# Performance work log

Hardware: AMD Instinct MI355X
Metric: run time of the kernel (lower is better)

Reference implementation:

```python
import jax, jax.numpy as jnp
import numpy as np

MARGIN = 0.3
PD_EPS = 1e-6  # torch F.pairwise_distance adds eps to the difference


def setup_inputs() -> dict:
    key = jax.random.key(0)
    k1, k2 = jax.random.split(key)
    B, D, NUM_CLASSES = 8192, 256, 8
    embeddings = jax.random.normal(k1, (B, D), dtype=jnp.float32)
    labels = jax.random.randint(k2, (B,), 0, NUM_CLASSES, dtype=jnp.int64)
    return {"embeddings": embeddings, "labels": labels}


def _pairwise_euclidean(x):
    # cdist(x, x, p=2) via the Gram trick; clamp tiny negatives before sqrt
    sq = jnp.sum(x * x, axis=1)  # [B]
    d2 = sq[:, None] + sq[None, :] - 2.0 * (x @ x.T)
    return jnp.sqrt(jnp.maximum(d2, 0.0))


def reference(embeddings, labels):
    B = embeddings.shape[0]
    D = _pairwise_euclidean(embeddings)  # [B, B]

    eq = labels[:, None] == labels[None, :]
    eye = jnp.eye(B, dtype=bool)
    pos_mask = eq & ~eye          # same label, not self
    neg_mask = ~eq                # different label

    # hard mining: per anchor, farthest positive and closest negative
    pos_idx = jnp.argmax(jnp.where(pos_mask, D, -jnp.inf), axis=1)  # [B]
    neg_idx = jnp.argmin(jnp.where(neg_mask, D, jnp.inf), axis=1)   # [B]
    valid = pos_mask.any(axis=1) & neg_mask.any(axis=1)             # [B]

    # recompute triplet distances like F.pairwise_distance (eps on the diff)
    pos_dist = jnp.linalg.norm(embeddings - embeddings[pos_idx] + PD_EPS, axis=1)
    neg_dist = jnp.linalg.norm(embeddings - embeddings[neg_idx] + PD_EPS, axis=1)

    per_anchor = jax.nn.relu(pos_dist - neg_dist + MARGIN)
    n_valid = jnp.maximum(valid.sum(), 1)
    loss = jnp.sum(jnp.where(valid, per_anchor, 0.0)) / n_valid.astype(per_anchor.dtype)
    return loss
```

## Files before the change

kernel.cpp:

```cpp
#include <hip/hip_runtime.h>
#include <math.h>


typedef __attribute__((ext_vector_type(8))) short short8;
typedef __attribute__((ext_vector_type(4))) float floatx4;

#define B_N 8192
#define D_K 256

__device__ __forceinline__ unsigned short f2bf_rne(float f) {
  unsigned u = __float_as_uint(f);
  u += 0x7FFFu + ((u >> 16) & 1u);
  return (unsigned short)(u >> 16);
}

#define DPP_SHR(x, CTRL) \
  ((unsigned)__builtin_amdgcn_update_dpp((int)(x), (int)(x), (CTRL), 0xF, 0xF, false))

__global__ void k_hist(const int* __restrict__ lab, int* __restrict__ chunkhist) {
  __shared__ int h[8];
  const int tid = threadIdx.x, b = blockIdx.x;
  if (tid < 8) h[tid] = 0;
  __syncthreads();
  atomicAdd(&h[lab[b * 256 + tid] & 7], 1);
  __syncthreads();
  if (tid < 8) chunkhist[b * 8 + tid] = h[tid];
}

__global__ void k_perm(const int* __restrict__ lab, const int* __restrict__ chunkhist,
                       int* __restrict__ perm, int* __restrict__ labp) {
  __shared__ int ch[256];
  __shared__ int base[8];
  __shared__ int wcnt[4][8];
  const int tid = threadIdx.x, b = blockIdx.x;
  ch[tid] = chunkhist[tid];
  __syncthreads();
  if (tid < 8) {
    const int c = tid;
    int acc = 0;
    for (int cc = 0; cc < c; ++cc)
      for (int k = 0; k < 32; ++k) acc += ch[k * 8 + cc];
    for (int k = 0; k < b; ++k) acc += ch[k * 8 + c];
    base[c] = acc;
  }
  const int i    = b * 256 + tid;
  const int myc  = lab[i] & 7;
  const int lane = tid & 63, w = tid >> 6;
  unsigned long long bal[8];
#pragma unroll
  for (int c = 0; c < 8; ++c) bal[c] = __ballot(myc == c);
  if (lane == 0) {
#pragma unroll
    for (int c = 0; c < 8; ++c) wcnt[w][c] = (int)__popcll(bal[c]);
  }
  __syncthreads();
  int rank = (int)__popcll(bal[myc] & ((1ull << lane) - 1ull));
  for (int ww = 0; ww < w; ++ww) rank += wcnt[ww][myc];
  const int pos = base[myc] + rank;
  perm[pos] = i;
  labp[pos] = myc;
}

__global__ void k_split(const float* __restrict__ x, const int* __restrict__ perm,
                        unsigned short* __restrict__ xhf,
                        float* __restrict__ sqq,
                        float* __restrict__ sum, int* __restrict__ cnt,
                        int* __restrict__ done) {
  __shared__ float sw[64];
  const int tid  = threadIdx.x;
  const int lane = tid & 63;
  const int w    = tid >> 6;
  const int b    = blockIdx.x;
  const int m    = lane & 15;
  const int quad = lane >> 4;
  const int row  = b * 16 + m;
  const int rsrc = perm[row];

  float s = 0.f;
#pragma unroll
  for (int h = 0; h < 2; ++h) {
    int tk = w + h * 4;
    int kk = tk * 32 + quad * 8;
    float4 f0 = *reinterpret_cast<const float4*>(x + (size_t)rsrc * D_K + kk);
    float4 f1 = *reinterpret_cast<const float4*>(x + (size_t)rsrc * D_K + kk + 4);
    s += f0.x * f0.x + f0.y * f0.y + f0.z * f0.z + f0.w * f0.w;
    s += f1.x * f1.x + f1.y * f1.y + f1.z * f1.z + f1.w * f1.w;
    ushort4 lo, hi;
    lo.x = f2bf_rne(f0.x); lo.y = f2bf_rne(f0.y); lo.z = f2bf_rne(f0.z); lo.w = f2bf_rne(f0.w);
    hi.x = f2bf_rne(f1.x); hi.y = f2bf_rne(f1.y); hi.z = f2bf_rne(f1.z); hi.w = f2bf_rne(f1.w);
    size_t o = ((size_t)b * 8 + tk) * 512 + lane * 8;
    *reinterpret_cast<ushort4*>(xhf + o)     = lo;
    *reinterpret_cast<ushort4*>(xhf + o + 4) = hi;
  }
  s += __shfl_xor(s, 16);
  s += __shfl_xor(s, 32);
  if (quad == 0) sw[w * 16 + m] = s;
  __syncthreads();
  if (tid < 16) {
    int i = b * 16 + tid;
    float t = sw[tid] + sw[16 + tid] + sw[32 + tid] + sw[48 + tid];
    sqq[i] = fmaf(t, 128.f, 262144.f);
  }
  if (b == 0 && tid == 0) { *sum = 0.f; *cnt = 0; *done = 0; }
}

template <int MODE>
__device__ __forceinline__ void mine_tail(
    const floatx4* acc, const int* __restrict__ labp, const float* __restrict__ sqq,
    int i0, int bi, int bj, int w, int lane,
    unsigned* jbp, unsigned* jbn,
    unsigned* __restrict__ ppart, unsigned* __restrict__ npart) {
  const int wj = w & 1;
  const int quad = lane >> 4, l15 = lane & 15;

  float sqi[16];
#pragma unroll
  for (int r = 0; r < 16; ++r)
    sqi[r] = sqq[i0 + (r >> 2) * 16 + quad * 4 + (r & 3)];

  unsigned long long lip = 0ull;
  if (MODE == 2) {
#pragma unroll
    for (int r = 0; r < 16; ++r) {
      int ir = i0 + (r >> 2) * 16 + quad * 4 + (r & 3);
      lip |= (unsigned long long)((unsigned)labp[ir] & 0xFu) << (r * 4);
    }
  }

  unsigned pkey[16], nkey[16];
#pragma unroll
  for (int r = 0; r < 16; ++r) { pkey[r] = 0u; nkey[r] = 0xFFFFFFFFu; }

#pragma unroll
  for (int nt = 0; nt < 4; ++nt) {
    const int      j  = bj * 128 + wj * 64 + nt * 16 + l15;
    const float    sj = sqq[j];
    const unsigned jl = (MODE == 2) ? ((unsigned)labp[j] & 0xFu) : 0u;
    unsigned jp = 0u, jn = 0xFFFFFFFFu;
#pragma unroll
    for (int r = 0; r < 16; ++r) {
      float dot = acc[(r >> 2) * 4 + nt][r & 3];
      int   ir  = i0 + (r >> 2) * 16 + quad * 4 + (r & 3);
      unsigned keyi = ((unsigned)fmaf(-256.f, dot, sj) << 13) | (unsigned)j;
      unsigned keyj = ((unsigned)fmaf(-256.f, dot, sqi[r]) << 13) | (unsigned)ir;
      if (MODE == 2) {
        bool eq = (jl == (unsigned)((lip >> (r * 4)) & 0xFull));
        unsigned pci = eq ? keyi : 0u;
        unsigned nci = eq ? 0xFFFFFFFFu : keyi;
        pkey[r] = pkey[r] > pci ? pkey[r] : pci;
        nkey[r] = nkey[r] < nci ? nkey[r] : nci;
        unsigned pcj = eq ? keyj : 0u;
        unsigned ncj = eq ? 0xFFFFFFFFu : keyj;
        jp = jp > pcj ? jp : pcj;
        jn = jn < ncj ? jn : ncj;
      } else if (MODE == 1) {
        pkey[r] = pkey[r] > keyi ? pkey[r] : keyi;
        jp = jp > keyj ? jp : keyj;
      } else {
        nkey[r] = nkey[r] < keyi ? nkey[r] : keyi;
        jn = jn < keyj ? jn : keyj;
      }
    }
#pragma unroll
    for (int m = 16; m < 64; m <<= 1) {
      if (MODE != 0) { unsigned op = (unsigned)__shfl_xor((int)jp, m); jp = jp > op ? jp : op; }
      if (MODE != 1) { unsigned on = (unsigned)__shfl_xor((int)jn, m); jn = jn < on ? jn : on; }
    }
    if (quad == 0) {
      if (MODE != 0) jbp[w * 64 + nt * 16 + l15] = jp;
      if (MODE != 1) jbn[w * 64 + nt * 16 + l15] = jn;
    }
  }

#pragma unroll
  for (int r = 0; r < 16; ++r) {
    if (MODE != 0) { unsigned tp = DPP_SHR(pkey[r], 0x118); pkey[r] = pkey[r] > tp ? pkey[r] : tp; }
    if (MODE != 1) { unsigned tn = DPP_SHR(nkey[r], 0x118); nkey[r] = nkey[r] < tn ? nkey[r] : tn; }
  }
#pragma unroll
  for (int r = 0; r < 16; ++r) {
    if (MODE != 0) { unsigned tp = DPP_SHR(pkey[r], 0x114); pkey[r] = pkey[r] > tp ? pkey[r] : tp; }
    if (MODE != 1) { unsigned tn = DPP_SHR(nkey[r], 0x114); nkey[r] = nkey[r] < tn ? nkey[r] : tn; }
  }
#pragma unroll
  for (int r = 0; r < 16; ++r) {
    if (MODE != 0) { unsigned tp = DPP_SHR(pkey[r], 0x112); pkey[r] = pkey[r] > tp ? pkey[r] : tp; }
    if (MODE != 1) { unsigned tn = DPP_SHR(nkey[r], 0x112); nkey[r] = nkey[r] < tn ? nkey[r] : tn; }
  }
#pragma unroll
  for (int r = 0; r < 16; ++r) {
    if (MODE != 0) { unsigned tp = DPP_SHR(pkey[r], 0x111); pkey[r] = pkey[r] > tp ? pkey[r] : tp; }
    if (MODE != 1) { unsigned tn = DPP_SHR(nkey[r], 0x111); nkey[r] = nkey[r] < tn ? nkey[r] : tn; }
  }
#pragma unroll
  for (int r = 0; r < 16; ++r) {
    if (l15 == 15) {
      int ir = i0 + (r >> 2) * 16 + quad * 4 + (r & 3);
      size_t idx = (size_t)(2 * bj + wj) * B_N + ir;
      ppart[idx] = (MODE == 0) ? 0u : pkey[r];
      npart[idx] = (MODE == 1) ? 0xFFFFFFFFu : nkey[r];
    }
  }

  __syncthreads();
  if ((w >> 1) == 0 && bi != bj) {
    unsigned p = 0u, n = 0xFFFFFFFFu;
    if (MODE != 0) {
      p = jbp[w * 64 + lane];
      unsigned p2 = jbp[(w + 2) * 64 + lane];
      p = p > p2 ? p : p2;
    }
    if (MODE != 1) {
      n = jbn[w * 64 + lane];
      unsigned n2 = jbn[(w + 2) * 64 + lane];
      n = n < n2 ? n : n2;
    }
    int j = bj * 128 + wj * 64 + lane;
    size_t v = (size_t)(2 * bi + wj)       * B_N + j;
    size_t u = (size_t)(2 * bi + (1 - wj)) * B_N + j;
    ppart[v] = p;   npart[v] = n;
    ppart[u] = 0u;  npart[u] = 0xFFFFFFFFu;
  }
}

__global__ __launch_bounds__(256, 3) void k_mine16(
    const unsigned short* __restrict__ xhf, const int* __restrict__ labp,
    const float* __restrict__ sqq,
    unsigned* __restrict__ ppart, unsigned* __restrict__ npart) {
  __shared__ unsigned jbp[4 * 64], jbn[4 * 64];

  int t  = blockIdx.x;
  int bi = (int)(64.5f - sqrtf(64.5f * 64.5f - 2.f * (float)t));
  int b0 = 64 * bi - (bi * (bi - 1)) / 2;
  if (t < b0) { bi--; b0 = 64 * bi - (bi * (bi - 1)) / 2; }
  else {
    int b1 = 64 * (bi + 1) - ((bi + 1) * bi) / 2;
    if (t >= b1) { bi++; b0 = b1; }
  }
  const int bj = bi + (t - b0);

  const int tid  = threadIdx.x;
  const int lane = tid & 63;
  const int w    = tid >> 6;
  const int wi   = w >> 1;
  const int wj   = w & 1;
  const int i0   = bi * 128 + wi * 64;

  const int la0 = labp[bi * 128];
  const int la1 = labp[bi * 128 + 127];
  const int lb0 = labp[bj * 128];
  const int lb1 = labp[bj * 128 + 127];

  const unsigned aoff = (unsigned)(bi * 8 + wi * 4) * 4096u + (unsigned)lane * 8u;
  const unsigned boff = (unsigned)(bj * 8 + wj * 4) * 4096u + (unsigned)lane * 8u;

  floatx4 acc[16];
#pragma unroll
  for (int q = 0; q < 16; ++q) acc[q] = (floatx4)0.f;

#pragma unroll
  for (int tk = 0; tk < 8; ++tk) {
    short8 Bf[4];
#pragma unroll
    for (int nt = 0; nt < 4; ++nt)
      Bf[nt] = *reinterpret_cast<const short8*>(xhf + boff + (unsigned)(nt * 4096 + tk * 512));
    short8 Af[4];
#pragma unroll
    for (int mt = 0; mt < 4; ++mt)
      Af[mt] = *reinterpret_cast<const short8*>(xhf + aoff + (unsigned)(mt * 4096 + tk * 512));
#pragma unroll
    for (int mt = 0; mt < 4; ++mt)
#pragma unroll
      for (int nt = 0; nt < 4; ++nt)
        acc[mt * 4 + nt] = __builtin_amdgcn_mfma_f32_16x16x32_bf16(
            Af[mt], Bf[nt], acc[mt * 4 + nt], 0, 0, 0);
  }

  if (la1 < lb0 || lb1 < la0) {
    mine_tail<0>(acc, labp, sqq, i0, bi, bj, w, lane, jbp, jbn, ppart, npart);
  } else if (la0 == lb1 && la1 == lb0) {
    mine_tail<1>(acc, labp, sqq, i0, bi, bj, w, lane, jbp, jbn, ppart, npart);
  } else {
    mine_tail<2>(acc, labp, sqq, i0, bi, bj, w, lane, jbp, jbn, ppart, npart);
  }
}

__global__ void k_finish(const float* __restrict__ x, const int* __restrict__ perm,
                         const unsigned* __restrict__ ppart,
                         const unsigned* __restrict__ npart,
                         float* __restrict__ sum, int* __restrict__ cnt,
                         int* __restrict__ done, float* __restrict__ out) {
  __shared__ unsigned spk[32], snk[32];
  __shared__ float ssum[4];
  __shared__ int   scnt[4];
  const int tid = threadIdx.x;
  const int a0  = blockIdx.x * 32;

  if (tid < 32) { spk[tid] = 0u; snk[tid] = 0xFFFFFFFFu; }
  __syncthreads();

  {
    const int a    = a0 + (tid & 31);
    const int part = tid >> 5;
    unsigned p = 0u, n = 0xFFFFFFFFu;
#pragma unroll
    for (int s = 0; s < 16; ++s) {
      size_t idx = (size_t)(part * 16 + s) * B_N + a;
      unsigned pv = ppart[idx];
      unsigned nv = npart[idx];
      p = p > pv ? p : pv;
      n = n < nv ? n : nv;
    }
    atomicMax(&spk[tid & 31], p);
    atomicMin(&snk[tid & 31], n);
  }
  __syncthreads();

  const int w = tid >> 6, lane = tid & 63;
  float lsum = 0.f; int lcnt = 0;
#pragma unroll
  for (int it = 0; it < 8; ++it) {
    int al = w * 8 + it;
    int a  = a0 + al;
    unsigned p = spk[al];
    unsigned n = snk[al];
    bool valid = (p != 0u) && (n != 0xFFFFFFFFu);
    int  pidx = valid ? (int)(p & 8191u) : 0;
    int  nidx = valid ? (int)(n & 8191u) : 0;
    int  ra = perm[a], rp = perm[pidx], rn = perm[nidx];

    float4 xa = *reinterpret_cast<const float4*>(x + (size_t)ra * D_K + lane * 4);
    float4 xp = *reinterpret_cast<const float4*>(x + (size_t)rp * D_K + lane * 4);
    float4 xn = *reinterpret_cast<const float4*>(x + (size_t)rn * D_K + lane * 4);
    float dx, sp = 0.f, sn = 0.f;
    dx = xa.x - xp.x + 1e-6f; sp = fmaf(dx, dx, sp);
    dx = xa.y - xp.y + 1e-6f; sp = fmaf(dx, dx, sp);
    dx = xa.z - xp.z + 1e-6f; sp = fmaf(dx, dx, sp);
    dx = xa.w - xp.w + 1e-6f; sp = fmaf(dx, dx, sp);
    dx = xa.x - xn.x + 1e-6f; sn = fmaf(dx, dx, sn);
    dx = xa.y - xn.y + 1e-6f; sn = fmaf(dx, dx, sn);
    dx = xa.z - xn.z + 1e-6f; sn = fmaf(dx, dx, sn);
    dx = xa.w - xn.w + 1e-6f; sn = fmaf(dx, dx, sn);
#pragma unroll
    for (int o = 32; o > 0; o >>= 1) {
      sp += __shfl_down(sp, o, 64);
      sn += __shfl_down(sn, o, 64);
    }
    if (lane == 0 && valid) {
      float per = sqrtf(sp) - sqrtf(sn) + 0.3f;
      if (per > 0.f) lsum += per;
      lcnt += 1;
    }
  }
  if (lane == 0) { ssum[w] = lsum; scnt[w] = lcnt; }
  __syncthreads();
  if (tid == 0) {
    atomicAdd(sum, ssum[0] + ssum[1] + ssum[2] + ssum[3]);
    atomicAdd(cnt, scnt[0] + scnt[1] + scnt[2] + scnt[3]);
    __threadfence();
    int prev = atomicAdd(done, 1);
    if (prev == gridDim.x - 1) {
      float s = atomicAdd(sum, 0.f);
      int   cc = atomicAdd(cnt, 0);
      if (cc < 1) cc = 1;
      out[0] = s / (float)cc;
    }
  }
}

extern "C" void kernel_launch(void* const* d_in, const int* in_sizes, int n_in,
                              void* d_out, int out_size, void* d_ws, size_t ws_size,
                              hipStream_t stream) {
  const float* x   = (const float*)d_in[0];
  const int*   lab = (const int*)d_in[1];
  float*       out = (float*)d_out;

  char* ws = (char*)d_ws;
  unsigned short* xhf = (unsigned short*)ws;
  int* perm      = (int*)(ws + (size_t)4096 * 1024);
  int* labp      = (int*)(ws + (size_t)4096 * 1024 + 32768);
  int* chunkhist = (int*)(ws + (size_t)4096 * 1024 + 65536);
  float* sqq = (float*)(ws + (size_t)4608 * 1024);
  char*  pb = ws + (size_t)4608 * 1024 + 65536;
  size_t seg = (size_t)128 * B_N * 4;
  unsigned* ppart = (unsigned*)(pb);
  unsigned* npart = (unsigned*)(pb + seg);
  float* sum  = (float*)(pb + 2 * seg);
  int*   cnt  = (int*)(sum + 1);
  int*   done = (int*)(sum + 2);

  k_hist<<<32, 256, 0, stream>>>(lab, chunkhist);
  k_perm<<<32, 256, 0, stream>>>(lab, chunkhist, perm, labp);
  k_split<<<B_N / 16, 256, 0, stream>>>(x, perm, xhf, sqq, sum, cnt, done);
  k_mine16<<<2080, 256, 0, stream>>>(xhf, labp, sqq, ppart, npart);
  k_finish<<<B_N / 32, 256, 0, stream>>>(x, perm, ppart, npart, sum, cnt, done, out);
}
```

Baseline: 118.4 us.

## Merge sort kernels, halve partial buffers, reduce tile halves in LDS, swizzle blocks

Replaces the two-kernel histogram/permutation pass with a single 1024-thread block doing a counting sort, which saves one launch and moves the accumulator reset there. In the mining kernel, the per-wave row partial results are first combined across the two column halves in shared memory. Each tile then writes one partial per row instead of two, halving the ppart/npart buffers and the reads in k_finish. Block indices are also remapped with a stride-260 swizzle to spread triangular tiles across CUs. The extra LDS buffers and the added barrier-phase reduction cost a little occupancy, and the sort now runs serially on one block.

```diff
diff --git a/kernel.cpp b/kernel.cpp
--- a/kernel.cpp
+++ b/kernel.cpp
@@ -17,55 +17,67 @@
 #define DPP_SHR(x, CTRL) \
   ((unsigned)__builtin_amdgcn_update_dpp((int)(x), (int)(x), (CTRL), 0xF, 0xF, false))
 
-__global__ void k_hist(const int* __restrict__ lab, int* __restrict__ chunkhist) {
-  __shared__ int h[8];
-  const int tid = threadIdx.x, b = blockIdx.x;
-  if (tid < 8) h[tid] = 0;
-  __syncthreads();
-  atomicAdd(&h[lab[b * 256 + tid] & 7], 1);
-  __syncthreads();
-  if (tid < 8) chunkhist[b * 8 + tid] = h[tid];
-}
-
-__global__ void k_perm(const int* __restrict__ lab, const int* __restrict__ chunkhist,
-                       int* __restrict__ perm, int* __restrict__ labp) {
-  __shared__ int ch[256];
-  __shared__ int base[8];
-  __shared__ int wcnt[4][8];
-  const int tid = threadIdx.x, b = blockIdx.x;
-  ch[tid] = chunkhist[tid];
+__global__ __launch_bounds__(1024) void k_sort(const int* __restrict__ lab,
+                                               int* __restrict__ perm,
+                                               int* __restrict__ labp,
+                                               float* __restrict__ sum,
+                                               int* __restrict__ cnt,
+                                               int* __restrict__ done) {
+  __shared__ int wtot[16][8];
+  __shared__ int wbase[16][8];
+  __shared__ int ctot[8];
+  __shared__ int cbase[8];
+  const int tid = threadIdx.x, lane = tid & 63, w = tid >> 6;
+
+  int l[8], pre[8];
+  int lcnt[8] = {0, 0, 0, 0, 0, 0, 0, 0};
+#pragma unroll
+  for (int k = 0; k < 8; ++k) {
+    l[k] = lab[tid * 8 + k] & 7;
+    pre[k] = lcnt[l[k]]++;
+  }
+  int v[8];
+#pragma unroll
+  for (int c = 0; c < 8; ++c) v[c] = lcnt[c];
+  for (int d = 1; d < 64; d <<= 1) {
+#pragma unroll
+    for (int c = 0; c < 8; ++c) {
+      int t = __shfl_up(v[c], d, 64);
+      if (lane >= d) v[c] += t;
+    }
+  }
+  int lex[8];
+#pragma unroll
+  for (int c = 0; c < 8; ++c) lex[c] = v[c] - lcnt[c];
+  if (lane == 63) {
+#pragma unroll
+    for (int c = 0; c < 8; ++c) wtot[w][c] = v[c];
+  }
   __syncthreads();
   if (tid < 8) {
-    const int c = tid;
     int acc = 0;
-    for (int cc = 0; cc < c; ++cc)
-      for (int k = 0; k < 32; ++k) acc += ch[k * 8 + cc];
-    for (int k = 0; k < b; ++k) acc += ch[k * 8 + c];
-    base[c] = acc;
-  }
-  const int i    = b * 256 + tid;
-  const int myc  = lab[i] & 7;
-  const int lane = tid & 63, w = tid >> 6;
-  unsigned long long bal[8];
-#pragma unroll
-  for (int c = 0; c < 8; ++c) bal[c] = __ballot(myc == c);
-  if (lane == 0) {
-#pragma unroll
-    for (int c = 0; c < 8; ++c) wcnt[w][c] = (int)__popcll(bal[c]);
-  }
-  __syncthreads();
-  int rank = (int)__popcll(bal[myc] & ((1ull << lane) - 1ull));
-  for (int ww = 0; ww < w; ++ww) rank += wcnt[ww][myc];
-  const int pos = base[myc] + rank;
-  perm[pos] = i;
-  labp[pos] = myc;
+    for (int ww = 0; ww < 16; ++ww) { wbase[ww][tid] = acc; acc += wtot[ww][tid]; }
+    ctot[tid] = acc;
+  }
+  __syncthreads();
+  if (tid == 0) {
+    int acc = 0;
+    for (int c = 0; c < 8; ++c) { cbase[c] = acc; acc += ctot[c]; }
+    *sum = 0.f; *cnt = 0; *done = 0;
+  }
+  __syncthreads();
+#pragma unroll
+  for (int k = 0; k < 8; ++k) {
+    int c = l[k];
+    int pos = cbase[c] + wbase[w][c] + lex[c] + pre[k];
+    perm[pos] = tid * 8 + k;
+    labp[pos] = c;
+  }
 }
 
 __global__ void k_split(const float* __restrict__ x, const int* __restrict__ perm,
                         unsigned short* __restrict__ xhf,
-                        float* __restrict__ sqq,
-                        float* __restrict__ sum, int* __restrict__ cnt,
-                        int* __restrict__ done) {
+                        float* __restrict__ sqq) {
   __shared__ float sw[64];
   const int tid  = threadIdx.x;
   const int lane = tid & 63;
@@ -101,14 +113,13 @@
     float t = sw[tid] + sw[16 + tid] + sw[32 + tid] + sw[48 + tid];
     sqq[i] = fmaf(t, 128.f, 262144.f);
   }
-  if (b == 0 && tid == 0) { *sum = 0.f; *cnt = 0; *done = 0; }
 }
 
 template <int MODE>
 __device__ __forceinline__ void mine_tail(
     const floatx4* acc, const int* __restrict__ labp, const float* __restrict__ sqq,
     int i0, int bi, int bj, int w, int lane,
-    unsigned* jbp, unsigned* jbn,
+    unsigned* jbp, unsigned* jbn, unsigned* ibp, unsigned* ibn,
     unsigned* __restrict__ ppart, unsigned* __restrict__ npart) {
   const int wj = w & 1;
   const int quad = lane >> 4, l15 = lane & 15;
@@ -167,8 +178,8 @@
       if (MODE != 1) { unsigned on = (unsigned)__shfl_xor((int)jn, m); jn = jn < on ? jn : on; }
     }
     if (quad == 0) {
-      if (MODE != 0) jbp[w * 64 + nt * 16 + l15] = jp;
-      if (MODE != 1) jbn[w * 64 + nt * 16 + l15] = jn;
+      jbp[w * 64 + nt * 16 + l15] = (MODE == 0) ? 0u : jp;
+      jbn[w * 64 + nt * 16 + l15] = (MODE == 1) ? 0xFFFFFFFFu : jn;
     }
   }
 
@@ -195,31 +206,37 @@
 #pragma unroll
   for (int r = 0; r < 16; ++r) {
     if (l15 == 15) {
-      int ir = i0 + (r >> 2) * 16 + quad * 4 + (r & 3);
-      size_t idx = (size_t)(2 * bj + wj) * B_N + ir;
-      ppart[idx] = (MODE == 0) ? 0u : pkey[r];
-      npart[idx] = (MODE == 1) ? 0xFFFFFFFFu : nkey[r];
-    }
-  }
-
-  __syncthreads();
-  if ((w >> 1) == 0 && bi != bj) {
-    unsigned p = 0u, n = 0xFFFFFFFFu;
-    if (MODE != 0) {
-      p = jbp[w * 64 + lane];
-      unsigned p2 = jbp[(w + 2) * 64 + lane];
-      p = p > p2 ? p : p2;
-    }
-    if (MODE != 1) {
-      n = jbn[w * 64 + lane];
-      unsigned n2 = jbn[(w + 2) * 64 + lane];
-      n = n < n2 ? n : n2;
-    }
-    int j = bj * 128 + wj * 64 + lane;
-    size_t v = (size_t)(2 * bi + wj)       * B_N + j;
-    size_t u = (size_t)(2 * bi + (1 - wj)) * B_N + j;
-    ppart[v] = p;   npart[v] = n;
-    ppart[u] = 0u;  npart[u] = 0xFFFFFFFFu;
+      int row = (r >> 2) * 16 + quad * 4 + (r & 3);
+      ibp[w * 64 + row] = (MODE == 0) ? 0u : pkey[r];
+      ibn[w * 64 + row] = (MODE == 1) ? 0xFFFFFFFFu : nkey[r];
+    }
+  }
+
+  __syncthreads();
+  if ((w & 1) == 0) {
+    const int half = w >> 1;
+    unsigned p  = ibp[(2 * half) * 64 + lane];
+    unsigned p2 = ibp[(2 * half + 1) * 64 + lane];
+    unsigned n  = ibn[(2 * half) * 64 + lane];
+    unsigned n2 = ibn[(2 * half + 1) * 64 + lane];
+    p = p > p2 ? p : p2;
+    n = n < n2 ? n : n2;
+    int ir = bi * 128 + half * 64 + lane;
+    size_t idx = (size_t)bj * B_N + ir;
+    ppart[idx] = p;
+    npart[idx] = n;
+  } else if (bi != bj) {
+    const int jh = w >> 1;
+    unsigned p  = jbp[jh * 64 + lane];
+    unsigned p2 = jbp[(jh + 2) * 64 + lane];
+    unsigned n  = jbn[jh * 64 + lane];
+    unsigned n2 = jbn[(jh + 2) * 64 + lane];
+    p = p > p2 ? p : p2;
+    n = n < n2 ? n : n2;
+    int j = bj * 128 + jh * 64 + lane;
+    size_t idx = (size_t)bi * B_N + j;
+    ppart[idx] = p;
+    npart[idx] = n;
   }
 }
 
@@ -228,8 +245,11 @@
     const float* __restrict__ sqq,
     unsigned* __restrict__ ppart, unsigned* __restrict__ npart) {
   __shared__ unsigned jbp[4 * 64], jbn[4 * 64];
-
-  int t  = blockIdx.x;
+  __shared__ unsigned ibp[4 * 64], ibn[4 * 64];
+
+  int t = blockIdx.x;
+  t = (t & 7) * 260 + (t >> 3);
+
   int bi = (int)(64.5f - sqrtf(64.5f * 64.5f - 2.f * (float)t));
   int b0 = 64 * bi - (bi * (bi - 1)) / 2;
   if (t < b0) { bi--; b0 = 64 * bi - (bi * (bi - 1)) / 2; }
@@ -277,11 +297,11 @@
   }
 
   if (la1 < lb0 || lb1 < la0) {
-    mine_tail<0>(acc, labp, sqq, i0, bi, bj, w, lane, jbp, jbn, ppart, npart);
+    mine_tail<0>(acc, labp, sqq, i0, bi, bj, w, lane, jbp, jbn, ibp, ibn, ppart, npart);
   } else if (la0 == lb1 && la1 == lb0) {
-    mine_tail<1>(acc, labp, sqq, i0, bi, bj, w, lane, jbp, jbn, ppart, npart);
+    mine_tail<1>(acc, labp, sqq, i0, bi, bj, w, lane, jbp, jbn, ibp, ibn, ppart, npart);
   } else {
-    mine_tail<2>(acc, labp, sqq, i0, bi, bj, w, lane, jbp, jbn, ppart, npart);
+    mine_tail<2>(acc, labp, sqq, i0, bi, bj, w, lane, jbp, jbn, ibp, ibn, ppart, npart);
   }
 }
 
@@ -304,8 +324,8 @@
     const int part = tid >> 5;
     unsigned p = 0u, n = 0xFFFFFFFFu;
 #pragma unroll
-    for (int s = 0; s < 16; ++s) {
-      size_t idx = (size_t)(part * 16 + s) * B_N + a;
+    for (int s = 0; s < 8; ++s) {
+      size_t idx = (size_t)(part * 8 + s) * B_N + a;
       unsigned pv = ppart[idx];
       unsigned nv = npart[idx];
       p = p > pv ? p : pv;
@@ -379,19 +399,17 @@
   unsigned short* xhf = (unsigned short*)ws;
   int* perm      = (int*)(ws + (size_t)4096 * 1024);
   int* labp      = (int*)(ws + (size_t)4096 * 1024 + 32768);
-  int* chunkhist = (int*)(ws + (size_t)4096 * 1024 + 65536);
   float* sqq = (float*)(ws + (size_t)4608 * 1024);
   char*  pb = ws + (size_t)4608 * 1024 + 65536;
-  size_t seg = (size_t)128 * B_N * 4;
+  size_t seg = (size_t)64 * B_N * 4;
   unsigned* ppart = (unsigned*)(pb);
   unsigned* npart = (unsigned*)(pb + seg);
   float* sum  = (float*)(pb + 2 * seg);
   int*   cnt  = (int*)(sum + 1);
   int*   done = (int*)(sum + 2);
 
-  k_hist<<<32, 256, 0, stream>>>(lab, chunkhist);
-  k_perm<<<32, 256, 0, stream>>>(lab, chunkhist, perm, labp);
-  k_split<<<B_N / 16, 256, 0, stream>>>(x, perm, xhf, sqq, sum, cnt, done);
+  k_sort<<<1, 1024, 0, stream>>>(lab, perm, labp, sum, cnt, done);
+  k_split<<<B_N / 16, 256, 0, stream>>>(x, perm, xhf, sqq);
   k_mine16<<<2080, 256, 0, stream>>>(xhf, labp, sqq, ppart, npart);
   k_finish<<<B_N / 32, 256, 0, stream>>>(x, perm, ppart, npart, sum, cnt, done, out);
 }
```

After: 121.0 us. 1.02x slower.

## Stage GEMM operands via async global-to-LDS double buffer and halve partial arrays

Applied to the files above, without the earlier changes.

The mining GEMM kernel now loads each block's A and B tiles cooperatively into a double-buffered LDS stage with global_load_lds, instead of every wave loading its fragments straight from global memory. Each bf16 fragment is fetched once per block rather than once per wave. The per-anchor partial max/min results are first reduced across the two column waves in shared memory, so each tile writes one slot instead of two. This halves the ppart/npart arrays and the reads in the finish kernel. The accumulator reset moves to the histogram kernel. The change adds about 32KB of LDS and a barrier per k-step, which may lower occupancy.

```diff
diff --git a/kernel.cpp b/kernel.cpp
--- a/kernel.cpp
+++ b/kernel.cpp
@@ -14,10 +14,18 @@
   return (unsigned short)(u >> 16);
 }
 
+__device__ __forceinline__ void gl_lds16(const unsigned short* g, unsigned short* l) {
+  __builtin_amdgcn_global_load_lds(
+      (const __attribute__((address_space(1))) unsigned int*)g,
+      (__attribute__((address_space(3))) unsigned int*)l, 16, 0, 0);
+}
+
 #define DPP_SHR(x, CTRL) \
   ((unsigned)__builtin_amdgcn_update_dpp((int)(x), (int)(x), (CTRL), 0xF, 0xF, false))
 
-__global__ void k_hist(const int* __restrict__ lab, int* __restrict__ chunkhist) {
+__global__ void k_hist(const int* __restrict__ lab, int* __restrict__ chunkhist,
+                       float* __restrict__ sum, int* __restrict__ cnt,
+                       int* __restrict__ done) {
   __shared__ int h[8];
   const int tid = threadIdx.x, b = blockIdx.x;
   if (tid < 8) h[tid] = 0;
@@ -25,6 +33,7 @@
   atomicAdd(&h[lab[b * 256 + tid] & 7], 1);
   __syncthreads();
   if (tid < 8) chunkhist[b * 8 + tid] = h[tid];
+  if (b == 0 && tid == 0) { *sum = 0.f; *cnt = 0; *done = 0; }
 }
 
 __global__ void k_perm(const int* __restrict__ lab, const int* __restrict__ chunkhist,
@@ -63,9 +72,7 @@
 
 __global__ void k_split(const float* __restrict__ x, const int* __restrict__ perm,
                         unsigned short* __restrict__ xhf,
-                        float* __restrict__ sqq,
-                        float* __restrict__ sum, int* __restrict__ cnt,
-                        int* __restrict__ done) {
+                        float* __restrict__ sqq) {
   __shared__ float sw[64];
   const int tid  = threadIdx.x;
   const int lane = tid & 63;
@@ -101,14 +108,13 @@
     float t = sw[tid] + sw[16 + tid] + sw[32 + tid] + sw[48 + tid];
     sqq[i] = fmaf(t, 128.f, 262144.f);
   }
-  if (b == 0 && tid == 0) { *sum = 0.f; *cnt = 0; *done = 0; }
 }
 
 template <int MODE>
 __device__ __forceinline__ void mine_tail(
     const floatx4* acc, const int* __restrict__ labp, const float* __restrict__ sqq,
     int i0, int bi, int bj, int w, int lane,
-    unsigned* jbp, unsigned* jbn,
+    unsigned* jbp, unsigned* jbn, unsigned* ibp, unsigned* ibn,
     unsigned* __restrict__ ppart, unsigned* __restrict__ npart) {
   const int wj = w & 1;
   const int quad = lane >> 4, l15 = lane & 15;
@@ -167,8 +173,8 @@
       if (MODE != 1) { unsigned on = (unsigned)__shfl_xor((int)jn, m); jn = jn < on ? jn : on; }
     }
     if (quad == 0) {
-      if (MODE != 0) jbp[w * 64 + nt * 16 + l15] = jp;
-      if (MODE != 1) jbn[w * 64 + nt * 16 + l15] = jn;
+      jbp[w * 64 + nt * 16 + l15] = (MODE == 0) ? 0u : jp;
+      jbn[w * 64 + nt * 16 + l15] = (MODE == 1) ? 0xFFFFFFFFu : jn;
     }
   }
 
@@ -195,31 +201,37 @@
 #pragma unroll
   for (int r = 0; r < 16; ++r) {
     if (l15 == 15) {
-      int ir = i0 + (r >> 2) * 16 + quad * 4 + (r & 3);
-      size_t idx = (size_t)(2 * bj + wj) * B_N + ir;
-      ppart[idx] = (MODE == 0) ? 0u : pkey[r];
-      npart[idx] = (MODE == 1) ? 0xFFFFFFFFu : nkey[r];
-    }
-  }
-
-  __syncthreads();
-  if ((w >> 1) == 0 && bi != bj) {
-    unsigned p = 0u, n = 0xFFFFFFFFu;
-    if (MODE != 0) {
-      p = jbp[w * 64 + lane];
-      unsigned p2 = jbp[(w + 2) * 64 + lane];
-      p = p > p2 ? p : p2;
-    }
-    if (MODE != 1) {
-      n = jbn[w * 64 + lane];
-      unsigned n2 = jbn[(w + 2) * 64 + lane];
-      n = n < n2 ? n : n2;
-    }
-    int j = bj * 128 + wj * 64 + lane;
-    size_t v = (size_t)(2 * bi + wj)       * B_N + j;
-    size_t u = (size_t)(2 * bi + (1 - wj)) * B_N + j;
-    ppart[v] = p;   npart[v] = n;
-    ppart[u] = 0u;  npart[u] = 0xFFFFFFFFu;
+      int row = (r >> 2) * 16 + quad * 4 + (r & 3);
+      ibp[w * 64 + row] = (MODE == 0) ? 0u : pkey[r];
+      ibn[w * 64 + row] = (MODE == 1) ? 0xFFFFFFFFu : nkey[r];
+    }
+  }
+
+  __syncthreads();
+  if ((w & 1) == 0) {
+    const int half = w >> 1;
+    unsigned p  = ibp[(2 * half) * 64 + lane];
+    unsigned p2 = ibp[(2 * half + 1) * 64 + lane];
+    unsigned n  = ibn[(2 * half) * 64 + lane];
+    unsigned n2 = ibn[(2 * half + 1) * 64 + lane];
+    p = p > p2 ? p : p2;
+    n = n < n2 ? n : n2;
+    int ir = bi * 128 + half * 64 + lane;
+    size_t idx = (size_t)bj * B_N + ir;
+    ppart[idx] = p;
+    npart[idx] = n;
+  } else if (bi != bj) {
+    const int jh = w >> 1;
+    unsigned p  = jbp[jh * 64 + lane];
+    unsigned p2 = jbp[(jh + 2) * 64 + lane];
+    unsigned n  = jbn[jh * 64 + lane];
+    unsigned n2 = jbn[(jh + 2) * 64 + lane];
+    p = p > p2 ? p : p2;
+    n = n < n2 ? n : n2;
+    int j = bj * 128 + jh * 64 + lane;
+    size_t idx = (size_t)bi * B_N + j;
+    ppart[idx] = p;
+    npart[idx] = n;
   }
 }
 
@@ -227,7 +239,9 @@
     const unsigned short* __restrict__ xhf, const int* __restrict__ labp,
     const float* __restrict__ sqq,
     unsigned* __restrict__ ppart, unsigned* __restrict__ npart) {
+  __shared__ unsigned short stage[2][16][512];
   __shared__ unsigned jbp[4 * 64], jbn[4 * 64];
+  __shared__ unsigned ibp[4 * 64], ibn[4 * 64];
 
   int t  = blockIdx.x;
   int bi = (int)(64.5f - sqrtf(64.5f * 64.5f - 2.f * (float)t));
@@ -251,37 +265,55 @@
   const int lb0 = labp[bj * 128];
   const int lb1 = labp[bj * 128 + 127];
 
-  const unsigned aoff = (unsigned)(bi * 8 + wi * 4) * 4096u + (unsigned)lane * 8u;
-  const unsigned boff = (unsigned)(bj * 8 + wj * 4) * 4096u + (unsigned)lane * 8u;
+  const unsigned short* srcA0 = xhf + (size_t)(bi * 8 + w)     * 4096 + lane * 8;
+  const unsigned short* srcA1 = xhf + (size_t)(bi * 8 + 4 + w) * 4096 + lane * 8;
+  const unsigned short* srcB0 = xhf + (size_t)(bj * 8 + w)     * 4096 + lane * 8;
+  const unsigned short* srcB1 = xhf + (size_t)(bj * 8 + 4 + w) * 4096 + lane * 8;
+
+#define STAGE(bf, tk)                                             \
+  do {                                                            \
+    gl_lds16(srcA0 + (tk) * 512, &stage[bf][w][0]);               \
+    gl_lds16(srcA1 + (tk) * 512, &stage[bf][4 + w][0]);           \
+    gl_lds16(srcB0 + (tk) * 512, &stage[bf][8 + w][0]);           \
+    gl_lds16(srcB1 + (tk) * 512, &stage[bf][12 + w][0]);          \
+  } while (0)
 
   floatx4 acc[16];
 #pragma unroll
   for (int q = 0; q < 16; ++q) acc[q] = (floatx4)0.f;
 
+  STAGE(0, 0);
+  __syncthreads();
+
+  int bf = 0;
 #pragma unroll
   for (int tk = 0; tk < 8; ++tk) {
+    if (tk < 7) STAGE(bf ^ 1, tk + 1);
     short8 Bf[4];
 #pragma unroll
     for (int nt = 0; nt < 4; ++nt)
-      Bf[nt] = *reinterpret_cast<const short8*>(xhf + boff + (unsigned)(nt * 4096 + tk * 512));
+      Bf[nt] = *reinterpret_cast<const short8*>(&stage[bf][8 + wj * 4 + nt][lane * 8]);
     short8 Af[4];
 #pragma unroll
     for (int mt = 0; mt < 4; ++mt)
-      Af[mt] = *reinterpret_cast<const short8*>(xhf + aoff + (unsigned)(mt * 4096 + tk * 512));
+      Af[mt] = *reinterpret_cast<const short8*>(&stage[bf][wi * 4 + mt][lane * 8]);
 #pragma unroll
     for (int mt = 0; mt < 4; ++mt)
 #pragma unroll
       for (int nt = 0; nt < 4; ++nt)
         acc[mt * 4 + nt] = __builtin_amdgcn_mfma_f32_16x16x32_bf16(
             Af[mt], Bf[nt], acc[mt * 4 + nt], 0, 0, 0);
-  }
+    __syncthreads();
+    bf ^= 1;
+  }
+#undef STAGE
 
   if (la1 < lb0 || lb1 < la0) {
-    mine_tail<0>(acc, labp, sqq, i0, bi, bj, w, lane, jbp, jbn, ppart, npart);
+    mine_tail<0>(acc, labp, sqq, i0, bi, bj, w, lane, jbp, jbn, ibp, ibn, ppart, npart);
   } else if (la0 == lb1 && la1 == lb0) {
-    mine_tail<1>(acc, labp, sqq, i0, bi, bj, w, lane, jbp, jbn, ppart, npart);
+    mine_tail<1>(acc, labp, sqq, i0, bi, bj, w, lane, jbp, jbn, ibp, ibn, ppart, npart);
   } else {
-    mine_tail<2>(acc, labp, sqq, i0, bi, bj, w, lane, jbp, jbn, ppart, npart);
+    mine_tail<2>(acc, labp, sqq, i0, bi, bj, w, lane, jbp, jbn, ibp, ibn, ppart, npart);
   }
 }
 
@@ -304,8 +336,8 @@
     const int part = tid >> 5;
     unsigned p = 0u, n = 0xFFFFFFFFu;
 #pragma unroll
-    for (int s = 0; s < 16; ++s) {
-      size_t idx = (size_t)(part * 16 + s) * B_N + a;
+    for (int s = 0; s < 8; ++s) {
+      size_t idx = (size_t)(part * 8 + s) * B_N + a;
       unsigned pv = ppart[idx];
       unsigned nv = npart[idx];
       p = p > pv ? p : pv;
@@ -382,16 +414,16 @@
   int* chunkhist = (int*)(ws + (size_t)4096 * 1024 + 65536);
   float* sqq = (float*)(ws + (size_t)4608 * 1024);
   char*  pb = ws + (size_t)4608 * 1024 + 65536;
-  size_t seg = (size_t)128 * B_N * 4;
+  size_t seg = (size_t)64 * B_N * 4;
   unsigned* ppart = (unsigned*)(pb);
   unsigned* npart = (unsigned*)(pb + seg);
   float* sum  = (float*)(pb + 2 * seg);
   int*   cnt  = (int*)(sum + 1);
   int*   done = (int*)(sum + 2);
 
-  k_hist<<<32, 256, 0, stream>>>(lab, chunkhist);
+  k_hist<<<32, 256, 0, stream>>>(lab, chunkhist, sum, cnt, done);
   k_perm<<<32, 256, 0, stream>>>(lab, chunkhist, perm, labp);
-  k_split<<<B_N / 16, 256, 0, stream>>>(x, perm, xhf, sqq, sum, cnt, done);
+  k_split<<<B_N / 16, 256, 0, stream>>>(x, perm, xhf, sqq);
   k_mine16<<<2080, 256, 0, stream>>>(xhf, labp, sqq, ppart, npart);
   k_finish<<<B_N / 32, 256, 0, stream>>>(x, perm, ppart, npart, sum, cnt, done, out);
 }
```

Result: faster. 114.7 us, median of 2 (-3.1%).
